# Kernel optimization log

Hardware: AMD Instinct MI355X
Metric: run time of the kernel (lower is better)

Reference implementation:

```python
import jax, jax.numpy as jnp
import numpy as np

N = 50000      # num nodes
E = 800000     # num edges
D = 64         # in_dim = hid_dim = out_dim
K = 8          # propagation hops (num_layers)
ALPHA = 0.6


def setup_inputs() -> dict:
    key = jax.random.key(0)
    ks = jax.random.split(key, 6)
    s = 1.0 / np.sqrt(D)
    return {
        "x": jax.random.normal(ks[0], (N, D), jnp.float32),
        "w_conv": jax.random.normal(ks[1], (D, D), jnp.float32) * s,
        "b_conv": jnp.zeros((D,), jnp.float32),
        "w1": jax.random.normal(ks[2], (D, D), jnp.float32) * s,
        "b1": jnp.zeros((D,), jnp.float32),
        "w2": jax.random.normal(ks[3], (D, D), jnp.float32) * s,
        "b2": jnp.zeros((D,), jnp.float32),
        "edge_index": jax.random.randint(ks[4], (2, E), 0, N, jnp.int64),
    }


def _gcn_norm(edge_index, num_nodes):
    # add self loops, symmetric normalization D^-1/2 (A+I) D^-1/2
    loop = jnp.arange(num_nodes, dtype=edge_index.dtype)
    src = jnp.concatenate([edge_index[0], loop])
    dst = jnp.concatenate([edge_index[1], loop])
    ones = jnp.ones(src.shape[0], jnp.float32)
    deg = jax.ops.segment_sum(ones, dst, num_segments=num_nodes)
    dinv = jnp.where(deg > 0, jax.lax.rsqrt(deg), 0.0)
    norm = dinv[src] * dinv[dst]  # [E+N]
    return src, dst, norm


def reference(x, w_conv, b_conv, w1, b1, w2, b2, edge_index):
    num_nodes = x.shape[0]
    src, dst, norm = _gcn_norm(edge_index, num_nodes)
    # SSGConv: h = alpha*x + (1-alpha)/K * sum_k A_hat^k x
    h = ALPHA * x
    xk = x
    coef = (1.0 - ALPHA) / K
    for _ in range(K):
        xk = jax.ops.segment_sum(norm[:, None] * xk[src], dst, num_segments=num_nodes)
        h = h + coef * xk
    h = h @ w_conv.T + b_conv        # SSGConv's internal Linear
    h = jax.nn.relu(h)               # F.relu(conv1(...))
    h = jax.nn.relu(h @ w1.T + b1)   # lin1 + relu (dropout p=0, eval)
    return h @ w2.T + b2             # lin2
```

## Files before the change

kernel.cpp:

```cpp
#include <hip/hip_runtime.h>

#define DD 64
#define ALPHA 0.6f
#define KHOPS 8
#define WP 72

typedef __attribute__((ext_vector_type(8))) short bf16x8;
typedef __attribute__((ext_vector_type(4))) float f32x4;

static __device__ __forceinline__ unsigned short f2bf(float f) {
    unsigned int u = __float_as_uint(f);
    unsigned int r = (u + 0x7FFFu + ((u >> 16) & 1u)) >> 16;
    return (unsigned short)r;
}
static __device__ __forceinline__ unsigned int pack2bf(float lo, float hi) {
    return (unsigned int)f2bf(lo) | ((unsigned int)f2bf(hi) << 16);
}

__global__ __launch_bounds__(256) void deg_count_kernel(const int* __restrict__ dst,
                                                        int* __restrict__ cnt, int e) {
    int i = blockIdx.x * blockDim.x + threadIdx.x;
    if (i < e) atomicAdd(&cnt[dst[i]], 1);
}

__global__ __launch_bounds__(256) void dinv_kernel(const int* __restrict__ cnt,
                                                   float2* __restrict__ dinvr, int n) {
    int i = blockIdx.x * blockDim.x + threadIdx.x;
    if (i < n) {
        float d = (float)(cnt[i] + 1);
        dinvr[i] = make_float2(rsqrtf(d), sqrtf(d));
    }
}

__global__ __launch_bounds__(256) void scan1_kernel(const int* __restrict__ cnt,
                                                    int* __restrict__ partials, int n) {
    int i = blockIdx.x * 256 + threadIdx.x;
    int v = (i < n) ? cnt[i] : 0;
    #pragma unroll
    for (int off = 1; off < 64; off <<= 1) v += __shfl_down(v, off, 64);
    __shared__ int ws[4];
    if ((threadIdx.x & 63) == 0) ws[threadIdx.x >> 6] = v;
    __syncthreads();
    if (threadIdx.x == 0) partials[blockIdx.x] = ws[0] + ws[1] + ws[2] + ws[3];
}

__global__ __launch_bounds__(1024) void scan2_kernel(int* __restrict__ partials, int nb) {
    __shared__ int s[1024];
    int t = threadIdx.x;
    int v = (t < nb) ? partials[t] : 0;
    s[t] = v;
    __syncthreads();
    for (int off = 1; off < 1024; off <<= 1) {
        int tmp = (t >= off) ? s[t - off] : 0;
        __syncthreads();
        s[t] += tmp;
        __syncthreads();
    }
    if (t < nb) partials[t] = s[t] - v;
}

__global__ __launch_bounds__(256) void scan3_kernel(const int* __restrict__ cnt,
                                                    const int* __restrict__ partials,
                                                    int* __restrict__ rowptr,
                                                    int* __restrict__ cursor, int n) {
    int t = threadIdx.x;
    int i = blockIdx.x * 256 + t;
    int v = (i < n) ? cnt[i] : 0;
    int lane = t & 63;
    int incl = v;
    #pragma unroll
    for (int off = 1; off < 64; off <<= 1) {
        int u = __shfl_up(incl, off, 64);
        if (lane >= off) incl += u;
    }
    __shared__ int wsum[4];
    if (lane == 63) wsum[t >> 6] = incl;
    __syncthreads();
    int woff = 0;
    for (int w = 0; w < (t >> 6); ++w) woff += wsum[w];
    int excl = incl - v + woff + partials[blockIdx.x];
    if (i < n) { rowptr[i] = excl; cursor[i] = excl; }
    if (i == n - 1) rowptr[n] = excl + v;
}

#define FCHUNK 2048
__global__ __launch_bounds__(256) void fill_kernel(const int* __restrict__ src,
                                                   const int* __restrict__ dst,
                                                   int* __restrict__ cursor,
                                                   int* __restrict__ esrc, int e, int n) {
    int xcd = blockIdx.x & 7;
    int chunk = blockIdx.x >> 3;
    int lo = (int)(((long long)n * xcd) >> 3);
    int hi = (int)(((long long)n * (xcd + 1)) >> 3);
    int base = chunk * FCHUNK + threadIdx.x * 8;
    if (base >= e) return;
    int4 s0 = *(const int4*)(src + base);
    int4 s1 = *(const int4*)(src + base + 4);
    int4 d0 = *(const int4*)(dst + base);
    int4 d1 = *(const int4*)(dst + base + 4);
    int sv[8] = {s0.x, s0.y, s0.z, s0.w, s1.x, s1.y, s1.z, s1.w};
    int dv[8] = {d0.x, d0.y, d0.z, d0.w, d1.x, d1.y, d1.z, d1.w};
    #pragma unroll
    for (int j = 0; j < 8; ++j) {
        if (base + j < e) {
            int d = dv[j];
            if (d >= lo && d < hi) {
                int pos = atomicAdd(&cursor[d], 1);
                esrc[pos] = sv[j];
            }
        }
    }
}

__global__ __launch_bounds__(256) void init_kernel(const float4* __restrict__ x,
                                                   const float2* __restrict__ dinvr,
                                                   float4* __restrict__ h,
                                                   ushort4* __restrict__ yb, int n4) {
    int i = blockIdx.x * blockDim.x + threadIdx.x;
    if (i >= n4) return;
    int row = i >> 4;
    float di = dinvr[row].x;
    float4 v = x[i];
    h[i] = make_float4(ALPHA * v.x, ALPHA * v.y, ALPHA * v.z, ALPHA * v.w);
    ushort4 b;
    b.x = f2bf(di * v.x); b.y = f2bf(di * v.y);
    b.z = f2bf(di * v.z); b.w = f2bf(di * v.w);
    yb[i] = b;
}

static __device__ __forceinline__ void add8(float* acc, uint4 v) {
    acc[0] += __uint_as_float(v.x << 16);
    acc[1] += __uint_as_float(v.x & 0xffff0000u);
    acc[2] += __uint_as_float(v.y << 16);
    acc[3] += __uint_as_float(v.y & 0xffff0000u);
    acc[4] += __uint_as_float(v.z << 16);
    acc[5] += __uint_as_float(v.z & 0xffff0000u);
    acc[6] += __uint_as_float(v.w << 16);
    acc[7] += __uint_as_float(v.w & 0xffff0000u);
}

template <int DO_H>
__global__ __launch_bounds__(256) void hop_kernel(const int* __restrict__ rowptr,
                                                  const int* __restrict__ esrc,
                                                  const float2* __restrict__ dinvr,
                                                  const unsigned short* __restrict__ yin,
                                                  unsigned short* __restrict__ yout,
                                                  float* __restrict__ h,
                                                  float coef, int n) {
    int wid = (blockIdx.x * blockDim.x + threadIdx.x) >> 6;
    if (wid >= n) return;
    int lane = threadIdx.x & 63;
    int g = lane >> 3;
    int s = lane & 7;
    int node = wid;

    int e0 = rowptr[node];
    int e1 = rowptr[node + 1];

    float acc[8] = {0.f, 0.f, 0.f, 0.f, 0.f, 0.f, 0.f, 0.f};
    float yprev[8];
    float2 dr;

    if (g == 0) {
        dr = dinvr[node];
        uint4 v = *(const uint4*)(yin + (size_t)node * 64 + s * 8);
        yprev[0] = __uint_as_float(v.x << 16);
        yprev[1] = __uint_as_float(v.x & 0xffff0000u);
        yprev[2] = __uint_as_float(v.y << 16);
        yprev[3] = __uint_as_float(v.y & 0xffff0000u);
        yprev[4] = __uint_as_float(v.z << 16);
        yprev[5] = __uint_as_float(v.z & 0xffff0000u);
        yprev[6] = __uint_as_float(v.w << 16);
        yprev[7] = __uint_as_float(v.w & 0xffff0000u);
        #pragma unroll
        for (int j = 0; j < 8; ++j) acc[j] = yprev[j];
    }

    int deg = e1 - e0;
    int niter = (deg + 7) >> 3;
    int clampe = e1 - 1;
    for (int i = 0; i < niter; i += 4) {
        int eA = e0 + (i << 3) + g;
        int eB = eA + 8, eC = eA + 16, eD = eA + 24;
        bool vA = eA < e1, vB = eB < e1, vC = eC < e1, vD = eD < e1;
        int sA = esrc[vA ? eA : clampe];
        int sB = esrc[vB ? eB : clampe];
        int sC = esrc[vC ? eC : clampe];
        int sD = esrc[vD ? eD : clampe];
        uint4 va = *(const uint4*)(yin + (size_t)sA * 64 + s * 8);
        uint4 vb = *(const uint4*)(yin + (size_t)sB * 64 + s * 8);
        uint4 vc = *(const uint4*)(yin + (size_t)sC * 64 + s * 8);
        uint4 vd = *(const uint4*)(yin + (size_t)sD * 64 + s * 8);
        if (!vA) va = make_uint4(0u, 0u, 0u, 0u);
        if (!vB) vb = make_uint4(0u, 0u, 0u, 0u);
        if (!vC) vc = make_uint4(0u, 0u, 0u, 0u);
        if (!vD) vd = make_uint4(0u, 0u, 0u, 0u);
        add8(acc, va);
        add8(acc, vb);
        add8(acc, vc);
        add8(acc, vd);
    }

    #pragma unroll
    for (int off = 8; off < 64; off <<= 1) {
        #pragma unroll
        for (int j = 0; j < 8; ++j) acc[j] += __shfl_xor(acc[j], off, 64);
    }

    if (g == 0) {
        float di = dr.x;
        float d2 = di * di;
        uint4 o;
        o.x = pack2bf(d2 * acc[0], d2 * acc[1]);
        o.y = pack2bf(d2 * acc[2], d2 * acc[3]);
        o.z = pack2bf(d2 * acc[4], d2 * acc[5]);
        o.w = pack2bf(d2 * acc[6], d2 * acc[7]);
        *(uint4*)(yout + (size_t)node * 64 + s * 8) = o;
        if (DO_H) {
            float rd = dr.y;
            float* hp = h + (size_t)node * 64 + s * 8;
            float4 h0 = *(float4*)hp;
            float4 h1 = *(float4*)(hp + 4);
            h0.x += coef * (rd * yprev[0] + di * acc[0]);
            h0.y += coef * (rd * yprev[1] + di * acc[1]);
            h0.z += coef * (rd * yprev[2] + di * acc[2]);
            h0.w += coef * (rd * yprev[3] + di * acc[3]);
            h1.x += coef * (rd * yprev[4] + di * acc[4]);
            h1.y += coef * (rd * yprev[5] + di * acc[5]);
            h1.z += coef * (rd * yprev[6] + di * acc[6]);
            h1.w += coef * (rd * yprev[7] + di * acc[7]);
            *(float4*)hp = h0;
            *(float4*)(hp + 4) = h1;
        }
    }
}

__global__ __launch_bounds__(256) void mlp_mfma_kernel(const float* __restrict__ hin,
                                                       const float* __restrict__ wc,
                                                       const float* __restrict__ bc,
                                                       const float* __restrict__ w1,
                                                       const float* __restrict__ b1,
                                                       const float* __restrict__ w2,
                                                       const float* __restrict__ b2,
                                                       float* __restrict__ out, int n) {
    __shared__ unsigned short wlds[3][64][WP];
    __shared__ unsigned short xlds[64][WP];
    int t = threadIdx.x;

    const float* wm[3] = {wc, w1, w2};
    #pragma unroll
    for (int m = 0; m < 3; ++m) {
        const float4* w4 = (const float4*)wm[m];
        #pragma unroll
        for (int k = 0; k < 4; ++k) {
            int fid = t + k * 256;
            int j = fid >> 4, c4 = fid & 15;
            float4 v = w4[fid];
            *(uint2*)&wlds[m][j][c4 * 4] =
                make_uint2(pack2bf(v.x, v.y), pack2bf(v.z, v.w));
        }
    }

    int r0 = blockIdx.x * 64;
    const float4* h4 = (const float4*)hin;
    #pragma unroll
    for (int k = 0; k < 4; ++k) {
        int fid = t + k * 256;
        int r = fid >> 4, c4 = fid & 15;
        int gr = r0 + r;
        float4 v = (gr < n) ? h4[(size_t)gr * 16 + c4]
                            : make_float4(0.f, 0.f, 0.f, 0.f);
        *(uint2*)&xlds[r][c4 * 4] = make_uint2(pack2bf(v.x, v.y), pack2bf(v.z, v.w));
    }
    __syncthreads();

    int lane = t & 63;
    int wv = t >> 6;
    int rbase = wv * 16;
    int lr = lane & 15;
    int kg = lane >> 4;
    const float* bias[3] = {bc, b1, b2};

    #pragma unroll
    for (int m = 0; m < 3; ++m) {
        bf16x8 a0 = *(bf16x8*)&xlds[rbase + lr][kg * 8];
        bf16x8 a1 = *(bf16x8*)&xlds[rbase + lr][32 + kg * 8];
        #pragma unroll
        for (int ct = 0; ct < 4; ++ct) {
            bf16x8 bv0 = *(bf16x8*)&wlds[m][ct * 16 + lr][kg * 8];
            bf16x8 bv1 = *(bf16x8*)&wlds[m][ct * 16 + lr][32 + kg * 8];
            f32x4 acc = {0.f, 0.f, 0.f, 0.f};
            acc = __builtin_amdgcn_mfma_f32_16x16x32_bf16(a0, bv0, acc, 0, 0, 0);
            acc = __builtin_amdgcn_mfma_f32_16x16x32_bf16(a1, bv1, acc, 0, 0, 0);
            float bb = bias[m][ct * 16 + lr];
            if (m < 2) {
                #pragma unroll
                for (int rg = 0; rg < 4; ++rg) {
                    float v = fmaxf(acc[rg] + bb, 0.0f);
                    xlds[rbase + kg * 4 + rg][ct * 16 + lr] = f2bf(v);
                }
            } else {
                #pragma unroll
                for (int rg = 0; rg < 4; ++rg) {
                    int gr = r0 + rbase + kg * 4 + rg;
                    if (gr < n) out[(size_t)gr * 64 + ct * 16 + lr] = acc[rg] + bb;
                }
            }
        }
    }
}

extern "C" void kernel_launch(void* const* d_in, const int* in_sizes, int n_in,
                              void* d_out, int out_size, void* d_ws, size_t ws_size,
                              hipStream_t stream) {
    const float* x      = (const float*)d_in[0];
    const float* w_conv = (const float*)d_in[1];
    const float* b_conv = (const float*)d_in[2];
    const float* w1     = (const float*)d_in[3];
    const float* b1     = (const float*)d_in[4];
    const float* w2     = (const float*)d_in[5];
    const float* b2     = (const float*)d_in[6];
    const int*   ei     = (const int*)d_in[7];

    int n = in_sizes[0] / DD;
    int e = in_sizes[7] / 2;
    const int* src = ei;
    const int* dst = ei + e;

    char* wsb = (char*)d_ws;
    int*    cnt      = (int*)(wsb + 0);
    float2* dinvr    = (float2*)(wsb + 256 * 1024);
    int*    rowptr   = (int*)(wsb + 768 * 1024);
    int*    cursor   = (int*)(wsb + 1024 * 1024);
    int*    partials = (int*)(wsb + 1280 * 1024);
    int*    esrc     = (int*)(wsb + 1344 * 1024);
    unsigned short* yb0 = (unsigned short*)(wsb + 1344 * 1024 + (size_t)e * 4);
    unsigned short* yb1 = yb0 + (size_t)n * DD;
    float* h = (float*)d_out;

    const int B = 256;
    int n4 = n * (DD / 4);
    int nb = (n + 255) / 256;

    hipMemsetAsync(cnt, 0, (size_t)n * sizeof(int), stream);
    deg_count_kernel<<<(e + B - 1) / B, B, 0, stream>>>(dst, cnt, e);
    dinv_kernel<<<(n + B - 1) / B, B, 0, stream>>>(cnt, dinvr, n);
    scan1_kernel<<<nb, B, 0, stream>>>(cnt, partials, n);
    scan2_kernel<<<1, 1024, 0, stream>>>(partials, nb);
    scan3_kernel<<<nb, B, 0, stream>>>(cnt, partials, rowptr, cursor, n);
    int nchunks = (e + FCHUNK - 1) / FCHUNK;
    fill_kernel<<<nchunks * 8, B, 0, stream>>>(src, dst, cursor, esrc, e, n);

    init_kernel<<<(n4 + B - 1) / B, B, 0, stream>>>(
        (const float4*)x, dinvr, (float4*)h, (ushort4*)yb0, n4);

    float coef = (1.0f - ALPHA) / (float)KHOPS;
    int hblocks = (int)(((size_t)n * 64 + B - 1) / B);

    unsigned short* cur = yb0;
    unsigned short* nxt = yb1;
    for (int k = 1; k <= KHOPS; ++k) {
        if (k % 2 == 0)
            hop_kernel<1><<<hblocks, B, 0, stream>>>(rowptr, esrc, dinvr, cur, nxt, h,
                                                     coef, n);
        else
            hop_kernel<0><<<hblocks, B, 0, stream>>>(rowptr, esrc, dinvr, cur, nxt, h,
                                                     coef, n);
        unsigned short* tmp = cur; cur = nxt; nxt = tmp;
    }

    mlp_mfma_kernel<<<(n + 63) / 64, B, 0, stream>>>(h, w_conv, b_conv, w1, b1,
                                                     w2, b2, (float*)d_out, n);
}
```

Measured before the change: 280.9 us.

## Partition degree atomics by XCD, fuse dinv into scan, skip final hop output

Degree counting now uses the same XCD-partitioned chunking as the fill kernel. Each block handles 2048 edges and only issues atomics for destinations in its XCD's node range, which improves L2 locality of the atomics. The separate dinv kernel is folded into scan1, and hipMemsetAsync is replaced by a small zero kernel. The last hop no longer writes its unused bf16 output. These changes remove one launch, some redundant memory traffic and contended atomics. In exchange, the dst array is read eight times by the degree kernel.

```diff
diff --git a/kernel.cpp b/kernel.cpp
--- a/kernel.cpp
+++ b/kernel.cpp
@@ -17,29 +17,47 @@
     return (unsigned int)f2bf(lo) | ((unsigned int)f2bf(hi) << 16);
 }
 
+__global__ __launch_bounds__(256) void zero_kernel(uint4* __restrict__ p, int n16) {
+    int i = blockIdx.x * blockDim.x + threadIdx.x;
+    if (i < n16) p[i] = make_uint4(0u, 0u, 0u, 0u);
+}
+
+#define FCHUNK 2048
 __global__ __launch_bounds__(256) void deg_count_kernel(const int* __restrict__ dst,
-                                                        int* __restrict__ cnt, int e) {
-    int i = blockIdx.x * blockDim.x + threadIdx.x;
-    if (i < e) atomicAdd(&cnt[dst[i]], 1);
-}
-
-__global__ __launch_bounds__(256) void dinv_kernel(const int* __restrict__ cnt,
-                                                   float2* __restrict__ dinvr, int n) {
-    int i = blockIdx.x * blockDim.x + threadIdx.x;
-    if (i < n) {
-        float d = (float)(cnt[i] + 1);
-        dinvr[i] = make_float2(rsqrtf(d), sqrtf(d));
+                                                        int* __restrict__ cnt,
+                                                        int e, int n) {
+    int xcd = blockIdx.x & 7;
+    int chunk = blockIdx.x >> 3;
+    int lo = (int)(((long long)n * xcd) >> 3);
+    int hi = (int)(((long long)n * (xcd + 1)) >> 3);
+    int base = chunk * FCHUNK + threadIdx.x * 8;
+    if (base >= e) return;
+    int4 d0 = *(const int4*)(dst + base);
+    int4 d1 = *(const int4*)(dst + base + 4);
+    int dv[8] = {d0.x, d0.y, d0.z, d0.w, d1.x, d1.y, d1.z, d1.w};
+    #pragma unroll
+    for (int j = 0; j < 8; ++j) {
+        if (base + j < e) {
+            int d = dv[j];
+            if (d >= lo && d < hi) atomicAdd(&cnt[d], 1);
+        }
     }
 }
 
 __global__ __launch_bounds__(256) void scan1_kernel(const int* __restrict__ cnt,
-                                                    int* __restrict__ partials, int n) {
+                                                    int* __restrict__ partials,
+                                                    float2* __restrict__ dinvr, int n) {
     int i = blockIdx.x * 256 + threadIdx.x;
     int v = (i < n) ? cnt[i] : 0;
-    #pragma unroll
-    for (int off = 1; off < 64; off <<= 1) v += __shfl_down(v, off, 64);
+    if (i < n) {
+        float d = (float)(v + 1);
+        dinvr[i] = make_float2(rsqrtf(d), sqrtf(d));
+    }
+    int sum = v;
+    #pragma unroll
+    for (int off = 1; off < 64; off <<= 1) sum += __shfl_down(sum, off, 64);
     __shared__ int ws[4];
-    if ((threadIdx.x & 63) == 0) ws[threadIdx.x >> 6] = v;
+    if ((threadIdx.x & 63) == 0) ws[threadIdx.x >> 6] = sum;
     __syncthreads();
     if (threadIdx.x == 0) partials[blockIdx.x] = ws[0] + ws[1] + ws[2] + ws[3];
 }
@@ -83,7 +101,6 @@
     if (i == n - 1) rowptr[n] = excl + v;
 }
 
-#define FCHUNK 2048
 __global__ __launch_bounds__(256) void fill_kernel(const int* __restrict__ src,
                                                    const int* __restrict__ dst,
                                                    int* __restrict__ cursor,
@@ -139,7 +156,7 @@
     acc[7] += __uint_as_float(v.w & 0xffff0000u);
 }
 
-template <int DO_H>
+template <int DO_H, int DO_OUT>
 __global__ __launch_bounds__(256) void hop_kernel(const int* __restrict__ rowptr,
                                                   const int* __restrict__ esrc,
                                                   const float2* __restrict__ dinvr,
@@ -210,12 +227,14 @@
     if (g == 0) {
         float di = dr.x;
         float d2 = di * di;
-        uint4 o;
-        o.x = pack2bf(d2 * acc[0], d2 * acc[1]);
-        o.y = pack2bf(d2 * acc[2], d2 * acc[3]);
-        o.z = pack2bf(d2 * acc[4], d2 * acc[5]);
-        o.w = pack2bf(d2 * acc[6], d2 * acc[7]);
-        *(uint4*)(yout + (size_t)node * 64 + s * 8) = o;
+        if (DO_OUT) {
+            uint4 o;
+            o.x = pack2bf(d2 * acc[0], d2 * acc[1]);
+            o.y = pack2bf(d2 * acc[2], d2 * acc[3]);
+            o.z = pack2bf(d2 * acc[4], d2 * acc[5]);
+            o.w = pack2bf(d2 * acc[6], d2 * acc[7]);
+            *(uint4*)(yout + (size_t)node * 64 + s * 8) = o;
+        }
         if (DO_H) {
             float rd = dr.y;
             float* hp = h + (size_t)node * 64 + s * 8;
@@ -341,14 +360,14 @@
     const int B = 256;
     int n4 = n * (DD / 4);
     int nb = (n + 255) / 256;
-
-    hipMemsetAsync(cnt, 0, (size_t)n * sizeof(int), stream);
-    deg_count_kernel<<<(e + B - 1) / B, B, 0, stream>>>(dst, cnt, e);
-    dinv_kernel<<<(n + B - 1) / B, B, 0, stream>>>(cnt, dinvr, n);
-    scan1_kernel<<<nb, B, 0, stream>>>(cnt, partials, n);
+    int nchunks = (e + FCHUNK - 1) / FCHUNK;
+
+    int n16 = (n + 3) / 4;
+    zero_kernel<<<(n16 + B - 1) / B, B, 0, stream>>>((uint4*)cnt, n16);
+    deg_count_kernel<<<nchunks * 8, B, 0, stream>>>(dst, cnt, e, n);
+    scan1_kernel<<<nb, B, 0, stream>>>(cnt, partials, dinvr, n);
     scan2_kernel<<<1, 1024, 0, stream>>>(partials, nb);
     scan3_kernel<<<nb, B, 0, stream>>>(cnt, partials, rowptr, cursor, n);
-    int nchunks = (e + FCHUNK - 1) / FCHUNK;
     fill_kernel<<<nchunks * 8, B, 0, stream>>>(src, dst, cursor, esrc, e, n);
 
     init_kernel<<<(n4 + B - 1) / B, B, 0, stream>>>(
@@ -360,12 +379,15 @@
     unsigned short* cur = yb0;
     unsigned short* nxt = yb1;
     for (int k = 1; k <= KHOPS; ++k) {
-        if (k % 2 == 0)
-            hop_kernel<1><<<hblocks, B, 0, stream>>>(rowptr, esrc, dinvr, cur, nxt, h,
-                                                     coef, n);
+        if (k == KHOPS)
+            hop_kernel<1, 0><<<hblocks, B, 0, stream>>>(rowptr, esrc, dinvr, cur, nxt,
+                                                        h, coef, n);
+        else if (k % 2 == 0)
+            hop_kernel<1, 1><<<hblocks, B, 0, stream>>>(rowptr, esrc, dinvr, cur, nxt,
+                                                        h, coef, n);
         else
-            hop_kernel<0><<<hblocks, B, 0, stream>>>(rowptr, esrc, dinvr, cur, nxt, h,
-                                                     coef, n);
+            hop_kernel<0, 1><<<hblocks, B, 0, stream>>>(rowptr, esrc, dinvr, cur, nxt,
+                                                        h, coef, n);
         unsigned short* tmp = cur; cur = nxt; nxt = tmp;
     }
 
```

Measured after the change: 277.7 us. About the same (-1.2%).
